# Kernel optimization log

Measured on AMD Instinct MI355X. Metric: run time of the kernel, lower is better.

The kernel has to match this reference:

```python
import jax, jax.numpy as jnp
import numpy as np

N = 50000        # nodes
E = 600000       # edges
D = 128          # hidden dim
FID = 128        # fixed_input_dim (one-hot size)
RWSE = 16        # rwse_dim
G = 128          # num graphs
L = 4            # num GIN blocks
DEG = 1001       # degree embedding table (clamp to 1000)
GIN_EPS = 0.0
BN_EPS = 1e-5


def setup_inputs() -> dict:
    key = jax.random.key(0)
    ks = jax.random.split(key, 16)
    s = 0.05
    inp = {
        "feat_id": jax.random.randint(ks[0], (N,), 0, 100000),
        "edge_index": jax.random.randint(ks[1], (2, E), 0, N),
        "batch_idx": jnp.sort(jax.random.randint(ks[2], (N,), 0, G)),
        "rwse": jax.random.normal(ks[3], (N, RWSE), jnp.float32),
        "in_degrees": jax.random.randint(ks[4], (N,), 0, DEG),
        # parameters
        "value_W": jax.random.normal(ks[5], (FID, D), jnp.float32) * s,
        "value_b": jnp.zeros((D,), jnp.float32),
        "rwse_W": jax.random.normal(ks[6], (RWSE, D), jnp.float32) * s,
        "rwse_b": jnp.zeros((D,), jnp.float32),
        "deg_emb": jax.random.normal(ks[7], (DEG, D), jnp.float32) * s,
        "mlp_W1": jax.random.normal(ks[8], (L, D, D), jnp.float32) * s,
        "mlp_b1": jnp.zeros((L, D), jnp.float32),
        "mlp_W2": jax.random.normal(ks[9], (L, D, D), jnp.float32) * s,
        "mlp_b2": jnp.zeros((L, D), jnp.float32),
        "bn_gamma": 1.0 + jax.random.normal(ks[10], (L, D), jnp.float32) * s,
        "bn_beta": jax.random.normal(ks[11], (L, D), jnp.float32) * s,
        "bn_mean": jax.random.normal(ks[12], (L, D), jnp.float32) * s,
        "bn_var": 1.0 + jax.random.uniform(ks[13], (L, D), jnp.float32) * 0.1,
    }
    return inp


def reference(feat_id, edge_index, batch_idx, rwse, in_degrees,
              value_W, value_b, rwse_W, rwse_b, deg_emb,
              mlp_W1, mlp_b1, mlp_W2, mlp_b2,
              bn_gamma, bn_beta, bn_mean, bn_var):
    # one_hot(feat_id % FID) @ value_W  ==  row gather of value_W
    h_id = jnp.remainder(feat_id, FID)
    h_attr = value_W[h_id] + value_b                      # [N, D]
    h_attr = h_attr + rwse @ rwse_W + rwse_b              # rwse projection
    deg = jnp.clip(in_degrees, 0, DEG - 1)
    h = h_attr + deg_emb[deg]                             # [N, D]

    src, dst = edge_index[0], edge_index[1]
    for l in range(L):
        # GIN aggregation: sum of neighbor messages + (1+eps)*self
        agg = jax.ops.segment_sum(h[src], dst, num_segments=N)
        agg = agg + (1.0 + GIN_EPS) * h
        # MLP: Linear -> ReLU -> Linear
        m = jax.nn.relu(agg @ mlp_W1[l] + mlp_b1[l]) @ mlp_W2[l] + mlp_b2[l]
        # BatchNorm (inference stats) + ReLU
        inv = bn_gamma[l] * jax.lax.rsqrt(bn_var[l] + BN_EPS)
        h = jax.nn.relu((m - bn_mean[l]) * inv + bn_beta[l])

    # scatter-mean graph pooling
    pooled = jax.ops.segment_sum(h, batch_idx, num_segments=G)      # [G, D]
    count = jax.ops.segment_sum(jnp.ones((N, 1), h.dtype), batch_idx,
                                num_segments=G)                     # [G, 1]
    graph_feature = pooled / jnp.maximum(count, 1.0)
    return graph_feature, h
```

## Files before the change

### kernel.cpp

```cpp
#include <hip/hip_runtime.h>

#define N_NODES 50000
#define N_EDGES 600000
#define DIM 128
#define NGRAPH 128
#define NLAYER 4
#define BN_EPS 1e-5f
#define SCAN_BLK 1024

#define EN_BLOCKS 3125
#define WT_BLOCKS 512
#define HB_BLOCKS 2344

using short8  = __attribute__((ext_vector_type(8))) short;
using float4v = __attribute__((ext_vector_type(4))) float;

__device__ __forceinline__ float bf2f(unsigned short u) {
    union { unsigned int i; float f; } c; c.i = ((unsigned int)u) << 16; return c.f;
}
__device__ __forceinline__ unsigned short f2bf(float f) {
    union { float f; unsigned int i; } c; c.f = f;
    unsigned int x = c.i;
    return (unsigned short)((x + 0x7fffu + ((x >> 16) & 1u)) >> 16);
}

__global__ void fused_pre_kernel(const int* __restrict__ feat_id,
                                 const float* __restrict__ rwse,
                                 const int* __restrict__ indeg,
                                 const float* __restrict__ value_W,
                                 const float* __restrict__ value_b,
                                 const float* __restrict__ rwse_W,
                                 const float* __restrict__ rwse_b,
                                 const float* __restrict__ deg_emb,
                                 unsigned short* __restrict__ hout,
                                 const float* __restrict__ W1,
                                 const float* __restrict__ W2,
                                 unsigned short* __restrict__ w1t,
                                 unsigned short* __restrict__ w2t,
                                 const int* __restrict__ dst,
                                 int* __restrict__ cnt)
{
    int b = blockIdx.x;
    if (b < EN_BLOCKS) {
        __shared__ float srw[16][16];
        __shared__ int   sfid[16], sdeg[16];
        const int t = threadIdx.x;
        const int base = b * 16;
        srw[t >> 4][t & 15] = rwse[(size_t)base * 16 + t];
        if (t < 16) sfid[t] = feat_id[base + t] & 127;
        else if (t < 32) {
            int dg = indeg[base + t - 16];
            sdeg[t - 16] = dg < 0 ? 0 : (dg > 1000 ? 1000 : dg);
        }
        const int d = t & 127, half = t >> 7;
        float wk[16];
#pragma unroll
        for (int k = 0; k < 16; ++k) wk[k] = rwse_W[k * DIM + d];
        float vb = value_b[d] + rwse_b[d];
        __syncthreads();
#pragma unroll
        for (int nn = 0; nn < 8; ++nn) {
            int nl = half * 8 + nn;
            int node = base + nl;
            float v = value_W[sfid[nl] * DIM + d] + vb + deg_emb[sdeg[nl] * DIM + d];
            float acc = 0.f;
#pragma unroll
            for (int k = 0; k < 16; ++k) acc += srw[nl][k] * wk[k];
            hout[(size_t)node * DIM + d] = f2bf(v + acc);
        }
    } else if (b < EN_BLOCKS + WT_BLOCKS) {
        int idx = (b - EN_BLOCKS) * 256 + threadIdx.x;
        int i = idx & (DIM * DIM - 1);
        int l = (idx >> 14) & 3;
        int is2 = idx >= NLAYER * DIM * DIM;
        int n = i >> 7, k = i & 127;
        const float* W = (is2 ? W2 : W1) + l * DIM * DIM;
        unsigned short v = f2bf(W[k * DIM + n]);
        (is2 ? w2t : w1t)[l * DIM * DIM + n * DIM + k] = v;
    } else {
        int e = (b - EN_BLOCKS - WT_BLOCKS) * 256 + threadIdx.x;
        if (e < N_EDGES) atomicAdd(&cnt[dst[e]], 1);
    }
}

__global__ void scanA_kernel(const int* __restrict__ cnt, int* __restrict__ rp, int* __restrict__ bsum) {
    __shared__ int sc[SCAN_BLK];
    int t = threadIdx.x, i = blockIdx.x * SCAN_BLK + t;
    int v = (i < N_NODES) ? cnt[i] : 0;
    sc[t] = v; __syncthreads();
    for (int off = 1; off < SCAN_BLK; off <<= 1) {
        int add = (t >= off) ? sc[t - off] : 0;
        __syncthreads();
        sc[t] += add;
        __syncthreads();
    }
    if (i < N_NODES) rp[i] = sc[t] - v;
    if (t == SCAN_BLK - 1) bsum[blockIdx.x] = sc[t];
}

__global__ void scan_fixup_kernel(int* __restrict__ rp, const int* __restrict__ bsum,
                                  int* __restrict__ cur, int nsb) {
    __shared__ int sbx[64];
    int t = threadIdx.x;
    if (t < 64) {
        int v = (t < nsb) ? bsum[t] : 0;
        int orig = v;
        for (int off = 1; off < 64; off <<= 1) {
            int y = __shfl_up(v, off, 64);
            if (t >= off) v += y;
        }
        sbx[t] = v - orig;
    }
    __syncthreads();
    int i = blockIdx.x * 256 + t;
    if (i < N_NODES) { int v = rp[i] + sbx[i >> 10]; rp[i] = v; cur[i] = v; }
    else if (i == N_NODES) rp[i] = N_EDGES;
}

__global__ void scatter_kernel(const int* __restrict__ src, const int* __restrict__ dst,
                               int* __restrict__ cur, int* __restrict__ esrc) {
    int e = blockIdx.x * blockDim.x + threadIdx.x;
    if (e < N_EDGES) {
        int pos = atomicAdd(&cur[dst[e]], 1);
        esrc[pos] = src[e];
    }
}

__global__ void __launch_bounds__(256) agg_kernel(const unsigned short* __restrict__ hin,
                                                  const int* __restrict__ rp,
                                                  const int* __restrict__ esrc,
                                                  unsigned short* __restrict__ aggout)
{
    int node = (blockIdx.x * blockDim.x + threadIdx.x) >> 6;
    node = __builtin_amdgcn_readfirstlane(node);
    if (node >= N_NODES) return;
    int lane = threadIdx.x & 63;
    int grp = lane >> 4, q = lane & 15;

    float a[8];
    if (grp == 0) {
        uint4 s = *(const uint4*)(hin + (size_t)node * DIM + q * 8);
        a[0] = bf2f((unsigned short)(s.x & 0xffff)); a[1] = bf2f((unsigned short)(s.x >> 16));
        a[2] = bf2f((unsigned short)(s.y & 0xffff)); a[3] = bf2f((unsigned short)(s.y >> 16));
        a[4] = bf2f((unsigned short)(s.z & 0xffff)); a[5] = bf2f((unsigned short)(s.z >> 16));
        a[6] = bf2f((unsigned short)(s.w & 0xffff)); a[7] = bf2f((unsigned short)(s.w >> 16));
    } else {
#pragma unroll
        for (int i = 0; i < 8; ++i) a[i] = 0.f;
    }

    int e1 = rp[node + 1];
    int e = rp[node] + grp;
    int snext = (e < e1) ? esrc[e] : 0;
    while (e < e1) {
        int s = snext;
        int en = e + 4;
        snext = (en < e1) ? esrc[en] : 0;
        uint4 v = *(const uint4*)(hin + (size_t)s * DIM + q * 8);
        a[0] += bf2f((unsigned short)(v.x & 0xffff)); a[1] += bf2f((unsigned short)(v.x >> 16));
        a[2] += bf2f((unsigned short)(v.y & 0xffff)); a[3] += bf2f((unsigned short)(v.y >> 16));
        a[4] += bf2f((unsigned short)(v.z & 0xffff)); a[5] += bf2f((unsigned short)(v.z >> 16));
        a[6] += bf2f((unsigned short)(v.w & 0xffff)); a[7] += bf2f((unsigned short)(v.w >> 16));
        e = en;
    }

#pragma unroll
    for (int i = 0; i < 8; ++i) {
        a[i] += __shfl_xor(a[i], 16, 64);
        a[i] += __shfl_xor(a[i], 32, 64);
    }

    if (grp == 0) {
        uint4 o;
        o.x = (unsigned int)f2bf(a[0]) | ((unsigned int)f2bf(a[1]) << 16);
        o.y = (unsigned int)f2bf(a[2]) | ((unsigned int)f2bf(a[3]) << 16);
        o.z = (unsigned int)f2bf(a[4]) | ((unsigned int)f2bf(a[5]) << 16);
        o.w = (unsigned int)f2bf(a[6]) | ((unsigned int)f2bf(a[7]) << 16);
        *(uint4*)(aggout + (size_t)node * DIM + q * 8) = o;
    }
}

__global__ void __launch_bounds__(64, 4) mlp_kernel(
    const unsigned short* __restrict__ aggin,
    const unsigned short* __restrict__ w1t,
    const unsigned short* __restrict__ w2t,
    const float* __restrict__ b1, const float* __restrict__ b2,
    const float* __restrict__ gam, const float* __restrict__ bet,
    const float* __restrict__ mean, const float* __restrict__ var,
    unsigned short* __restrict__ hout, float* __restrict__ fout, int last)
{
    __shared__ unsigned short sM[16 * DIM];
    const int lane = threadIdx.x;
    const int fr = lane & 15, fg = lane >> 4;
    const int rowbase = blockIdx.x * 16;

    const unsigned short* aptr = aggin + (size_t)(rowbase + fr) * DIM + fg * 8;
    short8 a0 = *(const short8*)(aptr);
    short8 a1 = *(const short8*)(aptr + 32);
    short8 a2 = *(const short8*)(aptr + 64);
    short8 a3 = *(const short8*)(aptr + 96);

    float4v acc[8];
#pragma unroll
    for (int n = 0; n < 8; ++n) acc[n] = (float4v){0.f, 0.f, 0.f, 0.f};

    const unsigned short* bp1 = w1t + fr * DIM + fg * 8;
#pragma unroll
    for (int nb = 0; nb < 8; ++nb) {
        const unsigned short* bb = bp1 + nb * 16 * DIM;
        short8 b0 = *(const short8*)(bb);
        short8 b1v = *(const short8*)(bb + 32);
        short8 b2v = *(const short8*)(bb + 64);
        short8 b3v = *(const short8*)(bb + 96);
        acc[nb] = __builtin_amdgcn_mfma_f32_16x16x32_bf16(a0, b0, acc[nb], 0, 0, 0);
        acc[nb] = __builtin_amdgcn_mfma_f32_16x16x32_bf16(a1, b1v, acc[nb], 0, 0, 0);
        acc[nb] = __builtin_amdgcn_mfma_f32_16x16x32_bf16(a2, b2v, acc[nb], 0, 0, 0);
        acc[nb] = __builtin_amdgcn_mfma_f32_16x16x32_bf16(a3, b3v, acc[nb], 0, 0, 0);
    }

#pragma unroll
    for (int nb = 0; nb < 8; ++nb) {
        int col = nb * 16 + fr;
        float bias = b1[col];
#pragma unroll
        for (int r = 0; r < 4; ++r) {
            int row = fg * 4 + r;
            float v = acc[nb][r] + bias;
            v = fmaxf(v, 0.f);
            int byte = row * 256 + col * 2; byte ^= (row & 7) << 4;
            *(unsigned short*)((char*)sM + byte) = f2bf(v);
        }
    }
    __syncthreads();

    short8 m0, m1, m2, m3;
    {
        int byte0 = fr * 256 + (fg * 8) * 2;       byte0 ^= (fr & 7) << 4;
        int byte1 = fr * 256 + (32 + fg * 8) * 2;  byte1 ^= (fr & 7) << 4;
        int byte2 = fr * 256 + (64 + fg * 8) * 2;  byte2 ^= (fr & 7) << 4;
        int byte3 = fr * 256 + (96 + fg * 8) * 2;  byte3 ^= (fr & 7) << 4;
        m0 = *(const short8*)((char*)sM + byte0);
        m1 = *(const short8*)((char*)sM + byte1);
        m2 = *(const short8*)((char*)sM + byte2);
        m3 = *(const short8*)((char*)sM + byte3);
    }

    float4v acc2[8];
#pragma unroll
    for (int n = 0; n < 8; ++n) acc2[n] = (float4v){0.f, 0.f, 0.f, 0.f};

    const unsigned short* bp2 = w2t + fr * DIM + fg * 8;
#pragma unroll
    for (int nb = 0; nb < 8; ++nb) {
        const unsigned short* bb = bp2 + nb * 16 * DIM;
        short8 b0 = *(const short8*)(bb);
        short8 b1v = *(const short8*)(bb + 32);
        short8 b2v = *(const short8*)(bb + 64);
        short8 b3v = *(const short8*)(bb + 96);
        acc2[nb] = __builtin_amdgcn_mfma_f32_16x16x32_bf16(m0, b0, acc2[nb], 0, 0, 0);
        acc2[nb] = __builtin_amdgcn_mfma_f32_16x16x32_bf16(m1, b1v, acc2[nb], 0, 0, 0);
        acc2[nb] = __builtin_amdgcn_mfma_f32_16x16x32_bf16(m2, b2v, acc2[nb], 0, 0, 0);
        acc2[nb] = __builtin_amdgcn_mfma_f32_16x16x32_bf16(m3, b3v, acc2[nb], 0, 0, 0);
    }

#pragma unroll
    for (int nb = 0; nb < 8; ++nb) {
        int col = nb * 16 + fr;
        float bias = b2[col];
        float iv = gam[col] * rsqrtf(var[col] + BN_EPS);
        float mn = mean[col], bt = bet[col];
#pragma unroll
        for (int r = 0; r < 4; ++r) {
            int node = rowbase + fg * 4 + r;
            float v = acc2[nb][r] + bias;
            v = (v - mn) * iv + bt;
            v = fmaxf(v, 0.f);
            if (last) fout[(size_t)node * DIM + col] = v;
            else hout[(size_t)node * DIM + col] = f2bf(v);
        }
    }
}

__global__ void __launch_bounds__(256) pool_partial_kernel(const float* __restrict__ h,
                                                           const int* __restrict__ batch,
                                                           float* __restrict__ partial)
{
    __shared__ float sums[256];
    __shared__ int sb[2];
    int g = blockIdx.x >> 3, split = blockIdx.x & 7;
    if (threadIdx.x < 2) {
        int target = g + threadIdx.x;
        int lo = 0, hi = N_NODES;
        while (lo < hi) { int mid = (lo + hi) >> 1; if (batch[mid] < target) lo = mid + 1; else hi = mid; }
        sb[threadIdx.x] = lo;
    }
    __syncthreads();
    int lo = sb[0], hi = sb[1];
    int d = threadIdx.x & 127, half = threadIdx.x >> 7;
    float acc = 0.f;
    for (int n = lo + split * 2 + half; n < hi; n += 16) acc += h[(size_t)n * DIM + d];
    sums[threadIdx.x] = acc;
    __syncthreads();
    if (threadIdx.x < 128)
        partial[blockIdx.x * DIM + threadIdx.x] = sums[threadIdx.x] + sums[threadIdx.x + 128];
}

__global__ void pool_comb_kernel(const float* __restrict__ partial,
                                 const int* __restrict__ batch,
                                 float* __restrict__ out)
{
    __shared__ int sb[2];
    int g = blockIdx.x, t = threadIdx.x;
    if (t < 2) {
        int target = g + t;
        int lo = 0, hi = N_NODES;
        while (lo < hi) { int mid = (lo + hi) >> 1; if (batch[mid] < target) lo = mid + 1; else hi = mid; }
        sb[t] = lo;
    }
    __syncthreads();
    float s = 0.f;
#pragma unroll
    for (int sp = 0; sp < 8; ++sp) s += partial[(g * 8 + sp) * DIM + t];
    float c = (float)(sb[1] - sb[0]);
    out[g * DIM + t] = s / fmaxf(c, 1.f);
}

extern "C" void kernel_launch(void* const* d_in, const int* in_sizes, int n_in,
                              void* d_out, int out_size, void* d_ws, size_t ws_size,
                              hipStream_t stream)
{
    const int*   feat_id = (const int*)d_in[0];
    const int*   eidx    = (const int*)d_in[1];
    const int*   batch   = (const int*)d_in[2];
    const float* rwse    = (const float*)d_in[3];
    const int*   indeg   = (const int*)d_in[4];
    const float* value_W = (const float*)d_in[5];
    const float* value_b = (const float*)d_in[6];
    const float* rwse_W  = (const float*)d_in[7];
    const float* rwse_b  = (const float*)d_in[8];
    const float* deg_emb = (const float*)d_in[9];
    const float* W1      = (const float*)d_in[10];
    const float* b1      = (const float*)d_in[11];
    const float* W2      = (const float*)d_in[12];
    const float* b2      = (const float*)d_in[13];
    const float* gam     = (const float*)d_in[14];
    const float* bet     = (const float*)d_in[15];
    const float* mean    = (const float*)d_in[16];
    const float* var     = (const float*)d_in[17];

    const int* srcv = eidx;
    const int* dstv = eidx + N_EDGES;

    char* p = (char*)d_ws;
    auto alloc = [&](size_t bytes) { char* r = p; p += (bytes + 255) & ~(size_t)255; return r; };
    unsigned short* hA   = (unsigned short*)alloc((size_t)N_NODES * DIM * 2);
    unsigned short* agg  = (unsigned short*)alloc((size_t)N_NODES * DIM * 2);
    int* cnt  = (int*)alloc((size_t)N_NODES * 4);
    int* rp   = (int*)alloc((size_t)(N_NODES + 1) * 4);
    int* cur  = (int*)alloc((size_t)N_NODES * 4);
    int* bsum = (int*)alloc(64 * 4);
    int* esrc = (int*)alloc((size_t)N_EDGES * 4);
    unsigned short* w1t = (unsigned short*)alloc((size_t)NLAYER * DIM * DIM * 2);
    unsigned short* w2t = (unsigned short*)alloc((size_t)NLAYER * DIM * DIM * 2);
    float* partial = (float*)alloc((size_t)NGRAPH * 8 * DIM * 4);

    float* out = (float*)d_out;
    float* hf  = out + NGRAPH * DIM;

    hipMemsetAsync(cnt, 0, (size_t)N_NODES * 4, stream);
    fused_pre_kernel<<<EN_BLOCKS + WT_BLOCKS + HB_BLOCKS, 256, 0, stream>>>(
        feat_id, rwse, indeg, value_W, value_b, rwse_W, rwse_b, deg_emb, hA,
        W1, W2, w1t, w2t, dstv, cnt);
    int nsb = (N_NODES + SCAN_BLK - 1) / SCAN_BLK;
    scanA_kernel<<<nsb, SCAN_BLK, 0, stream>>>(cnt, rp, bsum);
    scan_fixup_kernel<<<(N_NODES + 1 + 255) / 256, 256, 0, stream>>>(rp, bsum, cur, nsb);
    scatter_kernel<<<(N_EDGES + 255) / 256, 256, 0, stream>>>(srcv, dstv, cur, esrc);

    const int nrb = N_NODES / 16;
    for (int l = 0; l < NLAYER; ++l) {
        agg_kernel<<<(N_NODES * 64 + 255) / 256, 256, 0, stream>>>(hA, rp, esrc, agg);
        mlp_kernel<<<nrb, 64, 0, stream>>>(agg,
            w1t + l * DIM * DIM, w2t + l * DIM * DIM,
            b1 + l * DIM, b2 + l * DIM, gam + l * DIM, bet + l * DIM,
            mean + l * DIM, var + l * DIM,
            hA, hf, (l == NLAYER - 1) ? 1 : 0);
    }
    pool_partial_kernel<<<NGRAPH * 8, 256, 0, stream>>>(hf, batch, partial);
    pool_comb_kernel<<<NGRAPH, DIM, 0, stream>>>(partial, batch, out);
}
```

Measured before the change: 435.3 us.

## Fuse GIN neighbor aggregation into the MLP layer kernel via shared memory

Merges the separate aggregation and MLP kernels into one per-layer kernel. Each wave gathers and sums neighbor rows for 16 nodes one node at a time, stages the bf16 result in LDS, then runs both MFMA matmuls with BN and ReLU. Because a layer now reads and writes h in the same kernel, it ping-pongs between two h buffers. This removes the global round trip of the agg buffer and one launch per layer, but the gather loop runs serially over 16 nodes per wave, which lowers memory-level parallelism and may hurt latency hiding.

```diff
diff --git a/kernel.cpp b/kernel.cpp
--- a/kernel.cpp
+++ b/kernel.cpp
@@ -126,62 +126,10 @@
     }
 }
 
-__global__ void __launch_bounds__(256) agg_kernel(const unsigned short* __restrict__ hin,
-                                                  const int* __restrict__ rp,
-                                                  const int* __restrict__ esrc,
-                                                  unsigned short* __restrict__ aggout)
-{
-    int node = (blockIdx.x * blockDim.x + threadIdx.x) >> 6;
-    node = __builtin_amdgcn_readfirstlane(node);
-    if (node >= N_NODES) return;
-    int lane = threadIdx.x & 63;
-    int grp = lane >> 4, q = lane & 15;
-
-    float a[8];
-    if (grp == 0) {
-        uint4 s = *(const uint4*)(hin + (size_t)node * DIM + q * 8);
-        a[0] = bf2f((unsigned short)(s.x & 0xffff)); a[1] = bf2f((unsigned short)(s.x >> 16));
-        a[2] = bf2f((unsigned short)(s.y & 0xffff)); a[3] = bf2f((unsigned short)(s.y >> 16));
-        a[4] = bf2f((unsigned short)(s.z & 0xffff)); a[5] = bf2f((unsigned short)(s.z >> 16));
-        a[6] = bf2f((unsigned short)(s.w & 0xffff)); a[7] = bf2f((unsigned short)(s.w >> 16));
-    } else {
-#pragma unroll
-        for (int i = 0; i < 8; ++i) a[i] = 0.f;
-    }
-
-    int e1 = rp[node + 1];
-    int e = rp[node] + grp;
-    int snext = (e < e1) ? esrc[e] : 0;
-    while (e < e1) {
-        int s = snext;
-        int en = e + 4;
-        snext = (en < e1) ? esrc[en] : 0;
-        uint4 v = *(const uint4*)(hin + (size_t)s * DIM + q * 8);
-        a[0] += bf2f((unsigned short)(v.x & 0xffff)); a[1] += bf2f((unsigned short)(v.x >> 16));
-        a[2] += bf2f((unsigned short)(v.y & 0xffff)); a[3] += bf2f((unsigned short)(v.y >> 16));
-        a[4] += bf2f((unsigned short)(v.z & 0xffff)); a[5] += bf2f((unsigned short)(v.z >> 16));
-        a[6] += bf2f((unsigned short)(v.w & 0xffff)); a[7] += bf2f((unsigned short)(v.w >> 16));
-        e = en;
-    }
-
-#pragma unroll
-    for (int i = 0; i < 8; ++i) {
-        a[i] += __shfl_xor(a[i], 16, 64);
-        a[i] += __shfl_xor(a[i], 32, 64);
-    }
-
-    if (grp == 0) {
-        uint4 o;
-        o.x = (unsigned int)f2bf(a[0]) | ((unsigned int)f2bf(a[1]) << 16);
-        o.y = (unsigned int)f2bf(a[2]) | ((unsigned int)f2bf(a[3]) << 16);
-        o.z = (unsigned int)f2bf(a[4]) | ((unsigned int)f2bf(a[5]) << 16);
-        o.w = (unsigned int)f2bf(a[6]) | ((unsigned int)f2bf(a[7]) << 16);
-        *(uint4*)(aggout + (size_t)node * DIM + q * 8) = o;
-    }
-}
-
-__global__ void __launch_bounds__(64, 4) mlp_kernel(
-    const unsigned short* __restrict__ aggin,
+__global__ void __launch_bounds__(256, 4) layer_kernel(
+    const unsigned short* __restrict__ hin,
+    const int* __restrict__ rp,
+    const int* __restrict__ esrc,
     const unsigned short* __restrict__ w1t,
     const unsigned short* __restrict__ w2t,
     const float* __restrict__ b1, const float* __restrict__ b2,
@@ -189,16 +137,68 @@
     const float* __restrict__ mean, const float* __restrict__ var,
     unsigned short* __restrict__ hout, float* __restrict__ fout, int last)
 {
-    __shared__ unsigned short sM[16 * DIM];
-    const int lane = threadIdx.x;
+    __shared__ unsigned short sA[64 * DIM];
+    const int tid = threadIdx.x;
+    const int wave = tid >> 6, lane = tid & 63;
     const int fr = lane & 15, fg = lane >> 4;
-    const int rowbase = blockIdx.x * 16;
-
-    const unsigned short* aptr = aggin + (size_t)(rowbase + fr) * DIM + fg * 8;
-    short8 a0 = *(const short8*)(aptr);
-    short8 a1 = *(const short8*)(aptr + 32);
-    short8 a2 = *(const short8*)(aptr + 64);
-    short8 a3 = *(const short8*)(aptr + 96);
+    const int grp = fg, q = fr;
+    const int wrow0 = wave * 16;
+    const int rowbase = blockIdx.x * 64 + wrow0;
+
+    for (int j = 0; j < 16; ++j) {
+        int node = rowbase + j;
+        float a[8];
+#pragma unroll
+        for (int i = 0; i < 8; ++i) a[i] = 0.f;
+        if (node < N_NODES) {
+            if (grp == 0) {
+                uint4 s = *(const uint4*)(hin + (size_t)node * DIM + q * 8);
+                a[0] = bf2f((unsigned short)(s.x & 0xffff)); a[1] = bf2f((unsigned short)(s.x >> 16));
+                a[2] = bf2f((unsigned short)(s.y & 0xffff)); a[3] = bf2f((unsigned short)(s.y >> 16));
+                a[4] = bf2f((unsigned short)(s.z & 0xffff)); a[5] = bf2f((unsigned short)(s.z >> 16));
+                a[6] = bf2f((unsigned short)(s.w & 0xffff)); a[7] = bf2f((unsigned short)(s.w >> 16));
+            }
+            int e1 = rp[node + 1];
+            int e = rp[node] + grp;
+            int snext = (e < e1) ? esrc[e] : 0;
+            while (e < e1) {
+                int s = snext;
+                int en = e + 4;
+                snext = (en < e1) ? esrc[en] : 0;
+                uint4 v = *(const uint4*)(hin + (size_t)s * DIM + q * 8);
+                a[0] += bf2f((unsigned short)(v.x & 0xffff)); a[1] += bf2f((unsigned short)(v.x >> 16));
+                a[2] += bf2f((unsigned short)(v.y & 0xffff)); a[3] += bf2f((unsigned short)(v.y >> 16));
+                a[4] += bf2f((unsigned short)(v.z & 0xffff)); a[5] += bf2f((unsigned short)(v.z >> 16));
+                a[6] += bf2f((unsigned short)(v.w & 0xffff)); a[7] += bf2f((unsigned short)(v.w >> 16));
+                e = en;
+            }
+        }
+#pragma unroll
+        for (int i = 0; i < 8; ++i) {
+            a[i] += __shfl_xor(a[i], 16, 64);
+            a[i] += __shfl_xor(a[i], 32, 64);
+        }
+        if (grp == 0) {
+            uint4 o;
+            o.x = (unsigned int)f2bf(a[0]) | ((unsigned int)f2bf(a[1]) << 16);
+            o.y = (unsigned int)f2bf(a[2]) | ((unsigned int)f2bf(a[3]) << 16);
+            o.z = (unsigned int)f2bf(a[4]) | ((unsigned int)f2bf(a[5]) << 16);
+            o.w = (unsigned int)f2bf(a[6]) | ((unsigned int)f2bf(a[7]) << 16);
+            int row = wrow0 + j;
+            int byte = row * 256 + q * 16; byte ^= (row & 7) << 4;
+            *(uint4*)((char*)sA + byte) = o;
+        }
+    }
+
+    short8 a0, a1, a2, a3;
+    {
+        int row = wrow0 + fr;
+        int sw = (row & 7) << 4;
+        a0 = *(const short8*)((char*)sA + ((row * 256 + (0  + fg * 8) * 2) ^ sw));
+        a1 = *(const short8*)((char*)sA + ((row * 256 + (32 + fg * 8) * 2) ^ sw));
+        a2 = *(const short8*)((char*)sA + ((row * 256 + (64 + fg * 8) * 2) ^ sw));
+        a3 = *(const short8*)((char*)sA + ((row * 256 + (96 + fg * 8) * 2) ^ sw));
+    }
 
     float4v acc[8];
 #pragma unroll
@@ -224,25 +224,22 @@
         float bias = b1[col];
 #pragma unroll
         for (int r = 0; r < 4; ++r) {
-            int row = fg * 4 + r;
+            int row = wrow0 + fg * 4 + r;
             float v = acc[nb][r] + bias;
             v = fmaxf(v, 0.f);
             int byte = row * 256 + col * 2; byte ^= (row & 7) << 4;
-            *(unsigned short*)((char*)sM + byte) = f2bf(v);
-        }
-    }
-    __syncthreads();
+            *(unsigned short*)((char*)sA + byte) = f2bf(v);
+        }
+    }
 
     short8 m0, m1, m2, m3;
     {
-        int byte0 = fr * 256 + (fg * 8) * 2;       byte0 ^= (fr & 7) << 4;
-        int byte1 = fr * 256 + (32 + fg * 8) * 2;  byte1 ^= (fr & 7) << 4;
-        int byte2 = fr * 256 + (64 + fg * 8) * 2;  byte2 ^= (fr & 7) << 4;
-        int byte3 = fr * 256 + (96 + fg * 8) * 2;  byte3 ^= (fr & 7) << 4;
-        m0 = *(const short8*)((char*)sM + byte0);
-        m1 = *(const short8*)((char*)sM + byte1);
-        m2 = *(const short8*)((char*)sM + byte2);
-        m3 = *(const short8*)((char*)sM + byte3);
+        int row = wrow0 + fr;
+        int sw = (row & 7) << 4;
+        m0 = *(const short8*)((char*)sA + ((row * 256 + (0  + fg * 8) * 2) ^ sw));
+        m1 = *(const short8*)((char*)sA + ((row * 256 + (32 + fg * 8) * 2) ^ sw));
+        m2 = *(const short8*)((char*)sA + ((row * 256 + (64 + fg * 8) * 2) ^ sw));
+        m3 = *(const short8*)((char*)sA + ((row * 256 + (96 + fg * 8) * 2) ^ sw));
     }
 
     float4v acc2[8];
@@ -272,11 +269,13 @@
 #pragma unroll
         for (int r = 0; r < 4; ++r) {
             int node = rowbase + fg * 4 + r;
-            float v = acc2[nb][r] + bias;
-            v = (v - mn) * iv + bt;
-            v = fmaxf(v, 0.f);
-            if (last) fout[(size_t)node * DIM + col] = v;
-            else hout[(size_t)node * DIM + col] = f2bf(v);
+            if (node < N_NODES) {
+                float v = acc2[nb][r] + bias;
+                v = (v - mn) * iv + bt;
+                v = fmaxf(v, 0.f);
+                if (last) fout[(size_t)node * DIM + col] = v;
+                else hout[(size_t)node * DIM + col] = f2bf(v);
+            }
         }
     }
 }
@@ -354,7 +353,7 @@
     char* p = (char*)d_ws;
     auto alloc = [&](size_t bytes) { char* r = p; p += (bytes + 255) & ~(size_t)255; return r; };
     unsigned short* hA   = (unsigned short*)alloc((size_t)N_NODES * DIM * 2);
-    unsigned short* agg  = (unsigned short*)alloc((size_t)N_NODES * DIM * 2);
+    unsigned short* hB   = (unsigned short*)alloc((size_t)N_NODES * DIM * 2);
     int* cnt  = (int*)alloc((size_t)N_NODES * 4);
     int* rp   = (int*)alloc((size_t)(N_NODES + 1) * 4);
     int* cur  = (int*)alloc((size_t)N_NODES * 4);
@@ -376,14 +375,15 @@
     scan_fixup_kernel<<<(N_NODES + 1 + 255) / 256, 256, 0, stream>>>(rp, bsum, cur, nsb);
     scatter_kernel<<<(N_EDGES + 255) / 256, 256, 0, stream>>>(srcv, dstv, cur, esrc);
 
-    const int nrb = N_NODES / 16;
+    const int nlb = (N_NODES + 63) / 64;
     for (int l = 0; l < NLAYER; ++l) {
-        agg_kernel<<<(N_NODES * 64 + 255) / 256, 256, 0, stream>>>(hA, rp, esrc, agg);
-        mlp_kernel<<<nrb, 64, 0, stream>>>(agg,
+        const unsigned short* hi = (l & 1) ? hB : hA;
+        unsigned short*       ho = (l & 1) ? hA : hB;
+        layer_kernel<<<nlb, 256, 0, stream>>>(hi, rp, esrc,
             w1t + l * DIM * DIM, w2t + l * DIM * DIM,
             b1 + l * DIM, b2 + l * DIM, gam + l * DIM, bet + l * DIM,
             mean + l * DIM, var + l * DIM,
-            hA, hf, (l == NLAYER - 1) ? 1 : 0);
+            ho, hf, (l == NLAYER - 1) ? 1 : 0);
     }
     pool_partial_kernel<<<NGRAPH * 8, 256, 0, stream>>>(hf, batch, partial);
     pool_comb_kernel<<<NGRAPH, DIM, 0, stream>>>(partial, batch, out);
```

After: 506.3 us. +16.3%, slower.
